# Kernel optimization log

Hardware: AMD Instinct MI355X
Metric: run time of the kernel (lower is better)

## Reference

```python
import jax, jax.numpy as jnp
import numpy as np

T = 8388608  # sequence length (2^23)
WIDTH = 1.0


def phi(x, width=WIDTH):
    # Phi(x) = x if x > 0; x + width if x < -width; 0 otherwise
    return jnp.maximum(x, 0.0) + jnp.minimum(x + width, 0.0)


def setup_inputs() -> dict:
    key = jax.random.key(0)
    k1, k2 = jax.random.split(key)
    inputs = jax.random.normal(k1, (1, T), dtype=jnp.float32)
    state = jnp.zeros((1, 1), dtype=jnp.float32)
    # non_neg constrained scalar weight
    kernel = jax.random.uniform(k2, (1, 1), dtype=jnp.float32)
    return {"inputs": inputs, "state": state, "kernel": kernel}


def reference(inputs, state, kernel):
    # outputs_ = inputs * kernel (scalar multiply), then sequential hysteresis scan:
    #   out_i = Phi(outputs_[i] - out_{i-1}) + out_{i-1}
    xs = (inputs * kernel[0, 0])[0]  # [T]

    def step(prev, x):
        out = phi(x - prev) + prev
        return out, out

    last, outs = jax.lax.scan(step, state[0, 0], xs)
    outputs = outs.reshape(inputs.shape)       # [1, T]
    new_state = last.reshape(1, 1)             # [1, 1]
    return outputs, new_state
```

## Files before the change

kernel.cpp:

```cpp
#include <hip/hip_runtime.h>
#include <math.h>
#include <stdint.h>


#define TPB 256
#define WAVES 4
#define SEGS 4
#define FPL 8
#define SEG_ELEMS (TPB * FPL)
#define CHUNK_ELEMS (SEGS * SEG_ELEMS)
#define CHUNKS 4
#define BLK_ELEMS (CHUNKS * CHUNK_ELEMS)

typedef float v4f __attribute__((ext_vector_type(4)));

__device__ __forceinline__ float clampf(float x, float lo, float hi) {
    return fminf(fmaxf(x, lo), hi);
}
__device__ __forceinline__ uint64_t pack2(float lo, float hi) {
    union { float f[2]; uint64_t u; } u; u.f[0] = lo; u.f[1] = hi; return u.u;
}
__device__ __forceinline__ void unpack2(uint64_t w, float* lo, float* hi) {
    union { uint64_t u; float f[2]; } u; u.u = w; *lo = u.f[0]; *hi = u.f[1];
}

__global__ __launch_bounds__(TPB) void phi_scan(
    const v4f* __restrict__ x4,
    const float* __restrict__ kern,
    const float* __restrict__ state,
    float* __restrict__ out,
    uint64_t* __restrict__ agg,
    uint32_t* __restrict__ counter,
    int nblocks)
{
    __shared__ float wl[SEGS][WAVES], wh[SEGS][WAVES];
    __shared__ float rl[WAVES], rh[WAVES];
    __shared__ float s_v;

    const int t = threadIdx.x, lane = t & 63, w = t >> 6;
    const int b = blockIdx.x;
    const float k = kern[0];
    const size_t blk4 = (size_t)b * (BLK_ELEMS / 4);

    float bLo = -INFINITY, bHi = INFINITY;
    for (int c = 0; c < CHUNKS; ++c) {
        const size_t c4 = blk4 + (size_t)c * (CHUNK_ELEMS / 4);
        v4f v[SEGS][2];
#pragma unroll
        for (int s = 0; s < SEGS; ++s) {
            const size_t i4 = c4 + (size_t)s * (SEG_ELEMS / 4) + (size_t)t * 2;
            v[s][0] = x4[i4];
            v[s][1] = x4[i4 + 1];
        }
#pragma unroll
        for (int s = 0; s < SEGS; ++s) {
            float lo, hi, a;
            a = v[s][0].x * k; lo = a; hi = a + 1.0f;
            a = v[s][0].y * k; lo = clampf(lo, a, a + 1.0f); hi = clampf(hi, a, a + 1.0f);
            a = v[s][0].z * k; lo = clampf(lo, a, a + 1.0f); hi = clampf(hi, a, a + 1.0f);
            a = v[s][0].w * k; lo = clampf(lo, a, a + 1.0f); hi = clampf(hi, a, a + 1.0f);
            a = v[s][1].x * k; lo = clampf(lo, a, a + 1.0f); hi = clampf(hi, a, a + 1.0f);
            a = v[s][1].y * k; lo = clampf(lo, a, a + 1.0f); hi = clampf(hi, a, a + 1.0f);
            a = v[s][1].z * k; lo = clampf(lo, a, a + 1.0f); hi = clampf(hi, a, a + 1.0f);
            a = v[s][1].w * k; lo = clampf(lo, a, a + 1.0f); hi = clampf(hi, a, a + 1.0f);
#pragma unroll
            for (int off = 1; off < 64; off <<= 1) {
                float plo = __shfl_down(lo, off);
                float phi_ = __shfl_down(hi, off);
                float nlo = clampf(lo, plo, phi_);
                float nhi = clampf(hi, plo, phi_);
                lo = nlo; hi = nhi;
            }
            if (lane == 0) { wl[s][w] = lo; wh[s][w] = hi; }
        }
        __syncthreads();
        if (t == 0) {
#pragma unroll
            for (int s = 0; s < SEGS; ++s)
#pragma unroll
                for (int i = 0; i < WAVES; ++i) {
                    bLo = clampf(bLo, wl[s][i], wh[s][i]);
                    bHi = clampf(bHi, wl[s][i], wh[s][i]);
                }
        }
        __syncthreads();
    }

    if (t == 0) {
        __hip_atomic_store(&agg[b], pack2(bLo, bHi),
                           __ATOMIC_RELEASE, __HIP_MEMORY_SCOPE_AGENT);
        __hip_atomic_fetch_add(counter, 1u,
                               __ATOMIC_RELEASE, __HIP_MEMORY_SCOPE_AGENT);
    }
    __syncthreads();
    if (t == 0) {
        while (__hip_atomic_load(counter, __ATOMIC_ACQUIRE,
                                 __HIP_MEMORY_SCOPE_AGENT) < (uint32_t)nblocks)
            __builtin_amdgcn_s_sleep(16);
    }
    __syncthreads();

    {
        float lo = -INFINITY, hi = INFINITY;
        if (t < b) {
            float l, h;
            unpack2(__hip_atomic_load(&agg[t], __ATOMIC_RELAXED,
                                      __HIP_MEMORY_SCOPE_AGENT), &l, &h);
            lo = l; hi = h;
        }
#pragma unroll
        for (int off = 1; off < 64; off <<= 1) {
            float plo = __shfl_down(lo, off);
            float phi_ = __shfl_down(hi, off);
            float nlo = clampf(lo, plo, phi_);
            float nhi = clampf(hi, plo, phi_);
            lo = nlo; hi = nhi;
        }
        if (lane == 0) { rl[w] = lo; rh[w] = hi; }
        __syncthreads();
        if (t == 0) {
            float L = rl[0], H = rh[0];
#pragma unroll
            for (int i = 1; i < WAVES; ++i) {
                L = clampf(L, rl[i], rh[i]);
                H = clampf(H, rl[i], rh[i]);
            }
            s_v = clampf(state[0], L, H);
        }
        __syncthreads();
    }

    float p = s_v;
    for (int c = 0; c < CHUNKS; ++c) {
        const size_t c4 = blk4 + (size_t)c * (CHUNK_ELEMS / 4);
        float a[SEGS][FPL];
        float eslo[SEGS], eshi[SEGS], Slo[SEGS], Shi[SEGS];
#pragma unroll
        for (int s = 0; s < SEGS; ++s) {
            const size_t i4 = c4 + (size_t)s * (SEG_ELEMS / 4) + (size_t)t * 2;
            v4f v0 = __builtin_nontemporal_load(&x4[i4]);
            v4f v1 = __builtin_nontemporal_load(&x4[i4 + 1]);
            a[s][0] = v0.x * k; a[s][1] = v0.y * k; a[s][2] = v0.z * k; a[s][3] = v0.w * k;
            a[s][4] = v1.x * k; a[s][5] = v1.y * k; a[s][6] = v1.z * k; a[s][7] = v1.w * k;
            float lo = a[s][0], hi = a[s][0] + 1.0f;
#pragma unroll
            for (int j = 1; j < FPL; ++j) {
                lo = clampf(lo, a[s][j], a[s][j] + 1.0f);
                hi = clampf(hi, a[s][j], a[s][j] + 1.0f);
            }
#pragma unroll
            for (int off = 1; off < 64; off <<= 1) {
                float plo = __shfl_up(lo, off);
                float phi_ = __shfl_up(hi, off);
                if (lane >= off) {
                    float nlo = clampf(plo, lo, hi);
                    float nhi = clampf(phi_, lo, hi);
                    lo = nlo; hi = nhi;
                }
            }
            float elo = __shfl_up(lo, 1), ehi = __shfl_up(hi, 1);
            if (lane == 0) { elo = -INFINITY; ehi = INFINITY; }
            eslo[s] = elo; eshi[s] = ehi;
            if (lane == 63) { wl[s][w] = lo; wh[s][w] = hi; }
        }
        __syncthreads();
#pragma unroll
        for (int s = 0; s < SEGS; ++s) {
            float welo = -INFINITY, wehi = INFINITY;
            for (int i = 0; i < w; ++i) {
                welo = clampf(welo, wl[s][i], wh[s][i]);
                wehi = clampf(wehi, wl[s][i], wh[s][i]);
            }
            float llo = eslo[s], lhi = eshi[s];
            eslo[s] = clampf(welo, llo, lhi);
            eshi[s] = clampf(wehi, llo, lhi);
            float stl = -INFINITY, sth = INFINITY;
#pragma unroll
            for (int i = 0; i < WAVES; ++i) {
                stl = clampf(stl, wl[s][i], wh[s][i]);
                sth = clampf(sth, wl[s][i], wh[s][i]);
            }
            Slo[s] = stl; Shi[s] = sth;
        }
#pragma unroll
        for (int s = 0; s < SEGS; ++s) {
            float wv = clampf(p, eslo[s], eshi[s]);
            v4f r0, r1;
            wv = clampf(wv, a[s][0], a[s][0] + 1.0f); r0.x = wv;
            wv = clampf(wv, a[s][1], a[s][1] + 1.0f); r0.y = wv;
            wv = clampf(wv, a[s][2], a[s][2] + 1.0f); r0.z = wv;
            wv = clampf(wv, a[s][3], a[s][3] + 1.0f); r0.w = wv;
            wv = clampf(wv, a[s][4], a[s][4] + 1.0f); r1.x = wv;
            wv = clampf(wv, a[s][5], a[s][5] + 1.0f); r1.y = wv;
            wv = clampf(wv, a[s][6], a[s][6] + 1.0f); r1.z = wv;
            wv = clampf(wv, a[s][7], a[s][7] + 1.0f); r1.w = wv;
            v4f* o = (v4f*)(out + (size_t)b * BLK_ELEMS + (size_t)c * CHUNK_ELEMS
                            + (size_t)s * SEG_ELEMS) + (size_t)t * 2;
            __builtin_nontemporal_store(r0, &o[0]);
            __builtin_nontemporal_store(r1, &o[1]);
            p = clampf(p, Slo[s], Shi[s]);
        }
        __syncthreads();
    }

    if (b == nblocks - 1 && t == 0)
        out[(size_t)nblocks * BLK_ELEMS] = p;
}

extern "C" void kernel_launch(void* const* d_in, const int* in_sizes, int n_in,
                              void* d_out, int out_size, void* d_ws, size_t ws_size,
                              hipStream_t stream) {
    const v4f* x4      = (const v4f*)d_in[0];
    const float* state = (const float*)d_in[1];
    const float* kern  = (const float*)d_in[2];
    float* out = (float*)d_out;

    const size_t T = (size_t)in_sizes[0];
    const int nblocks = (int)(T / BLK_ELEMS);

    uint32_t* counter = (uint32_t*)d_ws;
    uint64_t* agg = (uint64_t*)((char*)d_ws + 16);

    hipMemsetAsync(d_ws, 0, 16, stream);
    phi_scan<<<nblocks, TPB, 0, stream>>>(x4, kern, state, out,
                                          agg, counter, nblocks);
}
```

Measured before the change: 118.0 us.

## Keep block data in registers across grid barrier to avoid re-reading input

```diff
diff --git a/kernel.cpp b/kernel.cpp
--- a/kernel.cpp
+++ b/kernel.cpp
@@ -8,9 +8,7 @@
 #define SEGS 4
 #define FPL 8
 #define SEG_ELEMS (TPB * FPL)
-#define CHUNK_ELEMS (SEGS * SEG_ELEMS)
-#define CHUNKS 4
-#define BLK_ELEMS (CHUNKS * CHUNK_ELEMS)
+#define BLK_ELEMS (SEGS * SEG_ELEMS)
 
 typedef float v4f __attribute__((ext_vector_type(4)));
 
@@ -24,7 +22,7 @@
     union { uint64_t u; float f[2]; } u; u.u = w; *lo = u.f[0]; *hi = u.f[1];
 }
 
-__global__ __launch_bounds__(TPB) void phi_scan(
+__global__ __launch_bounds__(TPB, 4) void phi_scan(
     const v4f* __restrict__ x4,
     const float* __restrict__ kern,
     const float* __restrict__ state,
@@ -42,58 +40,70 @@
     const float k = kern[0];
     const size_t blk4 = (size_t)b * (BLK_ELEMS / 4);
 
-    float bLo = -INFINITY, bHi = INFINITY;
-    for (int c = 0; c < CHUNKS; ++c) {
-        const size_t c4 = blk4 + (size_t)c * (CHUNK_ELEMS / 4);
-        v4f v[SEGS][2];
+    float a[SEGS][FPL];
+    float eslo[SEGS], eshi[SEGS];
+    float Slo[SEGS], Shi[SEGS];
+
 #pragma unroll
-        for (int s = 0; s < SEGS; ++s) {
-            const size_t i4 = c4 + (size_t)s * (SEG_ELEMS / 4) + (size_t)t * 2;
-            v[s][0] = x4[i4];
-            v[s][1] = x4[i4 + 1];
+    for (int s = 0; s < SEGS; ++s) {
+        const size_t i4 = blk4 + (size_t)s * (SEG_ELEMS / 4) + (size_t)t * 2;
+        v4f v0 = __builtin_nontemporal_load(&x4[i4]);
+        v4f v1 = __builtin_nontemporal_load(&x4[i4 + 1]);
+        a[s][0] = v0.x * k; a[s][1] = v0.y * k; a[s][2] = v0.z * k; a[s][3] = v0.w * k;
+        a[s][4] = v1.x * k; a[s][5] = v1.y * k; a[s][6] = v1.z * k; a[s][7] = v1.w * k;
+        float lo = a[s][0], hi = a[s][0] + 1.0f;
+#pragma unroll
+        for (int j = 1; j < FPL; ++j) {
+            lo = clampf(lo, a[s][j], a[s][j] + 1.0f);
+            hi = clampf(hi, a[s][j], a[s][j] + 1.0f);
         }
 #pragma unroll
-        for (int s = 0; s < SEGS; ++s) {
-            float lo, hi, a;
-            a = v[s][0].x * k; lo = a; hi = a + 1.0f;
-            a = v[s][0].y * k; lo = clampf(lo, a, a + 1.0f); hi = clampf(hi, a, a + 1.0f);
-            a = v[s][0].z * k; lo = clampf(lo, a, a + 1.0f); hi = clampf(hi, a, a + 1.0f);
-            a = v[s][0].w * k; lo = clampf(lo, a, a + 1.0f); hi = clampf(hi, a, a + 1.0f);
-            a = v[s][1].x * k; lo = clampf(lo, a, a + 1.0f); hi = clampf(hi, a, a + 1.0f);
-            a = v[s][1].y * k; lo = clampf(lo, a, a + 1.0f); hi = clampf(hi, a, a + 1.0f);
-            a = v[s][1].z * k; lo = clampf(lo, a, a + 1.0f); hi = clampf(hi, a, a + 1.0f);
-            a = v[s][1].w * k; lo = clampf(lo, a, a + 1.0f); hi = clampf(hi, a, a + 1.0f);
-#pragma unroll
-            for (int off = 1; off < 64; off <<= 1) {
-                float plo = __shfl_down(lo, off);
-                float phi_ = __shfl_down(hi, off);
-                float nlo = clampf(lo, plo, phi_);
-                float nhi = clampf(hi, plo, phi_);
+        for (int off = 1; off < 64; off <<= 1) {
+            float plo = __shfl_up(lo, off);
+            float phi_ = __shfl_up(hi, off);
+            if (lane >= off) {
+                float nlo = clampf(plo, lo, hi);
+                float nhi = clampf(phi_, lo, hi);
                 lo = nlo; hi = nhi;
             }
-            if (lane == 0) { wl[s][w] = lo; wh[s][w] = hi; }
         }
-        __syncthreads();
-        if (t == 0) {
+        float elo = __shfl_up(lo, 1), ehi = __shfl_up(hi, 1);
+        if (lane == 0) { elo = -INFINITY; ehi = INFINITY; }
+        eslo[s] = elo; eshi[s] = ehi;
+        if (lane == 63) { wl[s][w] = lo; wh[s][w] = hi; }
+    }
+    __syncthreads();
+
 #pragma unroll
-            for (int s = 0; s < SEGS; ++s)
+    for (int s = 0; s < SEGS; ++s) {
+        float welo = -INFINITY, wehi = INFINITY;
+        for (int i = 0; i < w; ++i) {
+            welo = clampf(welo, wl[s][i], wh[s][i]);
+            wehi = clampf(wehi, wl[s][i], wh[s][i]);
+        }
+        float llo = eslo[s], lhi = eshi[s];
+        eslo[s] = clampf(welo, llo, lhi);
+        eshi[s] = clampf(wehi, llo, lhi);
+        float stl = -INFINITY, sth = INFINITY;
 #pragma unroll
-                for (int i = 0; i < WAVES; ++i) {
-                    bLo = clampf(bLo, wl[s][i], wh[s][i]);
-                    bHi = clampf(bHi, wl[s][i], wh[s][i]);
-                }
+        for (int i = 0; i < WAVES; ++i) {
+            stl = clampf(stl, wl[s][i], wh[s][i]);
+            sth = clampf(sth, wl[s][i], wh[s][i]);
         }
-        __syncthreads();
+        Slo[s] = stl; Shi[s] = sth;
     }
 
     if (t == 0) {
-        __hip_atomic_store(&agg[b], pack2(bLo, bHi),
+        float Alo = -INFINITY, Ahi = INFINITY;
+#pragma unroll
+        for (int s = 0; s < SEGS; ++s) {
+            Alo = clampf(Alo, Slo[s], Shi[s]);
+            Ahi = clampf(Ahi, Slo[s], Shi[s]);
+        }
+        __hip_atomic_store(&agg[b], pack2(Alo, Ahi),
                            __ATOMIC_RELEASE, __HIP_MEMORY_SCOPE_AGENT);
         __hip_atomic_fetch_add(counter, 1u,
                                __ATOMIC_RELEASE, __HIP_MEMORY_SCOPE_AGENT);
-    }
-    __syncthreads();
-    if (t == 0) {
         while (__hip_atomic_load(counter, __ATOMIC_ACQUIRE,
                                  __HIP_MEMORY_SCOPE_AGENT) < (uint32_t)nblocks)
             __builtin_amdgcn_s_sleep(16);
@@ -101,12 +111,18 @@
     __syncthreads();
 
     {
+        const int per = nblocks / TPB;
         float lo = -INFINITY, hi = INFINITY;
-        if (t < b) {
-            float l, h;
-            unpack2(__hip_atomic_load(&agg[t], __ATOMIC_RELAXED,
-                                      __HIP_MEMORY_SCOPE_AGENT), &l, &h);
-            lo = l; hi = h;
+#pragma unroll
+        for (int c = 0; c < per; ++c) {
+            int j = t * per + c;
+            if (j < b) {
+                float l, h;
+                unpack2(__hip_atomic_load(&agg[j], __ATOMIC_RELAXED,
+                                          __HIP_MEMORY_SCOPE_AGENT), &l, &h);
+                lo = clampf(lo, l, h);
+                hi = clampf(hi, l, h);
+            }
         }
 #pragma unroll
         for (int off = 1; off < 64; off <<= 1) {
@@ -131,80 +147,28 @@
     }
 
     float p = s_v;
-    for (int c = 0; c < CHUNKS; ++c) {
-        const size_t c4 = blk4 + (size_t)c * (CHUNK_ELEMS / 4);
-        float a[SEGS][FPL];
-        float eslo[SEGS], eshi[SEGS], Slo[SEGS], Shi[SEGS];
+    float wv = p;
 #pragma unroll
-        for (int s = 0; s < SEGS; ++s) {
-            const size_t i4 = c4 + (size_t)s * (SEG_ELEMS / 4) + (size_t)t * 2;
-            v4f v0 = __builtin_nontemporal_load(&x4[i4]);
-            v4f v1 = __builtin_nontemporal_load(&x4[i4 + 1]);
-            a[s][0] = v0.x * k; a[s][1] = v0.y * k; a[s][2] = v0.z * k; a[s][3] = v0.w * k;
-            a[s][4] = v1.x * k; a[s][5] = v1.y * k; a[s][6] = v1.z * k; a[s][7] = v1.w * k;
-            float lo = a[s][0], hi = a[s][0] + 1.0f;
-#pragma unroll
-            for (int j = 1; j < FPL; ++j) {
-                lo = clampf(lo, a[s][j], a[s][j] + 1.0f);
-                hi = clampf(hi, a[s][j], a[s][j] + 1.0f);
-            }
-#pragma unroll
-            for (int off = 1; off < 64; off <<= 1) {
-                float plo = __shfl_up(lo, off);
-                float phi_ = __shfl_up(hi, off);
-                if (lane >= off) {
-                    float nlo = clampf(plo, lo, hi);
-                    float nhi = clampf(phi_, lo, hi);
-                    lo = nlo; hi = nhi;
-                }
-            }
-            float elo = __shfl_up(lo, 1), ehi = __shfl_up(hi, 1);
-            if (lane == 0) { elo = -INFINITY; ehi = INFINITY; }
-            eslo[s] = elo; eshi[s] = ehi;
-            if (lane == 63) { wl[s][w] = lo; wh[s][w] = hi; }
-        }
-        __syncthreads();
-#pragma unroll
-        for (int s = 0; s < SEGS; ++s) {
-            float welo = -INFINITY, wehi = INFINITY;
-            for (int i = 0; i < w; ++i) {
-                welo = clampf(welo, wl[s][i], wh[s][i]);
-                wehi = clampf(wehi, wl[s][i], wh[s][i]);
-            }
-            float llo = eslo[s], lhi = eshi[s];
-            eslo[s] = clampf(welo, llo, lhi);
-            eshi[s] = clampf(wehi, llo, lhi);
-            float stl = -INFINITY, sth = INFINITY;
-#pragma unroll
-            for (int i = 0; i < WAVES; ++i) {
-                stl = clampf(stl, wl[s][i], wh[s][i]);
-                sth = clampf(sth, wl[s][i], wh[s][i]);
-            }
-            Slo[s] = stl; Shi[s] = sth;
-        }
-#pragma unroll
-        for (int s = 0; s < SEGS; ++s) {
-            float wv = clampf(p, eslo[s], eshi[s]);
-            v4f r0, r1;
-            wv = clampf(wv, a[s][0], a[s][0] + 1.0f); r0.x = wv;
-            wv = clampf(wv, a[s][1], a[s][1] + 1.0f); r0.y = wv;
-            wv = clampf(wv, a[s][2], a[s][2] + 1.0f); r0.z = wv;
-            wv = clampf(wv, a[s][3], a[s][3] + 1.0f); r0.w = wv;
-            wv = clampf(wv, a[s][4], a[s][4] + 1.0f); r1.x = wv;
-            wv = clampf(wv, a[s][5], a[s][5] + 1.0f); r1.y = wv;
-            wv = clampf(wv, a[s][6], a[s][6] + 1.0f); r1.z = wv;
-            wv = clampf(wv, a[s][7], a[s][7] + 1.0f); r1.w = wv;
-            v4f* o = (v4f*)(out + (size_t)b * BLK_ELEMS + (size_t)c * CHUNK_ELEMS
-                            + (size_t)s * SEG_ELEMS) + (size_t)t * 2;
-            __builtin_nontemporal_store(r0, &o[0]);
-            __builtin_nontemporal_store(r1, &o[1]);
-            p = clampf(p, Slo[s], Shi[s]);
-        }
-        __syncthreads();
+    for (int s = 0; s < SEGS; ++s) {
+        wv = clampf(p, eslo[s], eshi[s]);
+        v4f r0, r1;
+        wv = clampf(wv, a[s][0], a[s][0] + 1.0f); r0.x = wv;
+        wv = clampf(wv, a[s][1], a[s][1] + 1.0f); r0.y = wv;
+        wv = clampf(wv, a[s][2], a[s][2] + 1.0f); r0.z = wv;
+        wv = clampf(wv, a[s][3], a[s][3] + 1.0f); r0.w = wv;
+        wv = clampf(wv, a[s][4], a[s][4] + 1.0f); r1.x = wv;
+        wv = clampf(wv, a[s][5], a[s][5] + 1.0f); r1.y = wv;
+        wv = clampf(wv, a[s][6], a[s][6] + 1.0f); r1.z = wv;
+        wv = clampf(wv, a[s][7], a[s][7] + 1.0f); r1.w = wv;
+        v4f* o = (v4f*)(out + (size_t)b * BLK_ELEMS + (size_t)s * SEG_ELEMS)
+                 + (size_t)t * 2;
+        __builtin_nontemporal_store(r0, &o[0]);
+        __builtin_nontemporal_store(r1, &o[1]);
+        p = clampf(p, Slo[s], Shi[s]);
     }
 
-    if (b == nblocks - 1 && t == 0)
-        out[(size_t)nblocks * BLK_ELEMS] = p;
+    if (b == nblocks - 1 && t == TPB - 1)
+        out[(size_t)nblocks * BLK_ELEMS] = wv;
 }
 
 extern "C" void kernel_launch(void* const* d_in, const int* in_sizes, int n_in,
```

Result: slower. 186.0 us (+57.6%).
